# Performance work log

Measured on AMD Instinct MI355X. Metric: run time of the kernel, lower is better.

The kernel has to match this reference:

```python
import jax, jax.numpy as jnp
import numpy as np

B, S, D, H = 2, 2048, 1024, 16
HD = D // H
SCALING = HD ** -0.5


def _length_mask(lengths, seqlen):
    return (jnp.arange(seqlen)[None, :] < jnp.asarray(lengths)[:, None]).astype(jnp.int32)


def setup_inputs() -> dict:
    key = jax.random.key(0)
    ks = jax.random.split(key, 10)
    std = D ** -0.5
    inp = {
        "hidden_states": jax.random.normal(ks[0], (B, S, D), dtype=jnp.float32),
        "Wq": jax.random.normal(ks[1], (D, D), dtype=jnp.float32) * std,
        "bq": jax.random.normal(ks[2], (D,), dtype=jnp.float32) * 0.02,
        "Wk": jax.random.normal(ks[3], (D, D), dtype=jnp.float32) * std,
        "bk": jax.random.normal(ks[4], (D,), dtype=jnp.float32) * 0.02,
        "Wv": jax.random.normal(ks[5], (D, D), dtype=jnp.float32) * std,
        "bv": jax.random.normal(ks[6], (D,), dtype=jnp.float32) * 0.02,
        "Wo": jax.random.normal(ks[7], (D, D), dtype=jnp.float32) * std,
        "bo": jax.random.normal(ks[8], (D,), dtype=jnp.float32) * 0.02,
        # variable valid lengths per batch element (padding at the end)
        "query_mask_1d": _length_mask([S, S - 512], S),
        "key_mask_1d": _length_mask([S, S - 512], S),
    }
    return inp


def reference(hidden_states, Wq, bq, Wk, bk, Wv, bv, Wo, bo, query_mask_1d, key_mask_1d):
    bsz, tgt_len, _ = hidden_states.shape
    # projections (dropout p=0 / eval -> identity)
    q = (hidden_states @ Wq + bq) * SCALING
    k = hidden_states @ Wk + bk
    v = hidden_states @ Wv + bv
    q = q.reshape(bsz, tgt_len, H, HD).transpose(0, 2, 1, 3)  # [B,H,S,HD]
    k = k.reshape(bsz, -1, H, HD).transpose(0, 2, 1, 3)
    v = v.reshape(bsz, -1, H, HD).transpose(0, 2, 1, 3)

    scores = jnp.einsum("bhqd,bhkd->bhqk", q, k)  # [B,H,S,S]
    q_valid = (query_mask_1d != 0)[:, None, :, None]  # [B,1,S,1]
    k_valid = (key_mask_1d != 0)[:, None, None, :]    # [B,1,1,S]
    # masked_fill(-inf) on padded keys; padded-query rows would be all -inf ->
    # softmax NaN -> nan_to_num(0). We compute the same result NaN-free by
    # zeroing the scores of padded-query rows and zeroing their probs after.
    s = jnp.where(k_valid, scores, -jnp.inf)
    s = jnp.where(q_valid, s, 0.0)
    attn_weights = jax.nn.softmax(s, axis=-1) * q_valid  # == softmax + nan_to_num

    attn_output = jnp.einsum("bhqk,bhkd->bhqd", attn_weights, v)
    attn_output = attn_output.transpose(0, 2, 1, 3).reshape(bsz, tgt_len, D)
    attn_output = attn_output @ Wo + bo
    return attn_output
```

## Files before the change

### kernel.cpp

```cpp
#include <hip/hip_runtime.h>
#include <stdint.h>

#define BB 2
#define SS 2048
#define DD 1024
#define HH 16
#define HDIM 64
#define MTOT (BB*SS)
#define QK_SCALE_LOG2E 0.180336880f

typedef unsigned short u16;
typedef __attribute__((ext_vector_type(8))) __bf16 bf16x8;
typedef __attribute__((ext_vector_type(4))) float f32x4;

static __device__ __forceinline__ float exp2_hw(float x) {
    return __builtin_amdgcn_exp2f(x);
}

static __device__ __forceinline__ u16 f2bu(float f) {
    union { float f; uint32_t u; } c; c.f = f;
    uint32_t u = c.u + 0x7fffu + ((c.u >> 16) & 1u);
    return (u16)(u >> 16);
}

static __device__ __forceinline__ u16 f2b_hw(float f) {
    __bf16 b = (__bf16)f;
    union { __bf16 b; u16 u; } c; c.b = b;
    return c.u;
}

static __device__ __forceinline__ uint32_t cvt_pk_bf16(float lo, float hi) {
    uint32_t r;
    asm("v_cvt_pk_bf16_f32 %0, %1, %2" : "=v"(r) : "v"(lo), "v"(hi));
    return r;
}

static __device__ __forceinline__ void gload_lds16(const void* g, void* l) {
    __builtin_amdgcn_global_load_lds(
        (const __attribute__((address_space(1))) uint32_t*)(g),
        (__attribute__((address_space(3))) uint32_t*)(l),
        16, 0, 0);
}

__global__ void k_convert_x(const float* __restrict__ x, u16* __restrict__ xb) {
    int i = (blockIdx.x * blockDim.x + threadIdx.x) * 4;
    float4 v = *(const float4*)(x + i);
    ushort4 o;
    o.x = f2bu(v.x); o.y = f2bu(v.y); o.z = f2bu(v.z); o.w = f2bu(v.w);
    *(ushort4*)(xb + i) = o;
}

__global__ void k_transpose_w(const float* __restrict__ Wq, const float* __restrict__ Wk,
                              const float* __restrict__ Wv, const float* __restrict__ Wo,
                              u16* __restrict__ Wqkv_t, u16* __restrict__ Wo_t) {
    __shared__ float tile[32][33];
    const int which = blockIdx.z;
    const float* W = (which == 0) ? Wq : (which == 1) ? Wk : (which == 2) ? Wv : Wo;
    u16* dst = (which < 3) ? (Wqkv_t + (size_t)which * DD * DD) : Wo_t;
    const int n0 = blockIdx.x * 32, k0 = blockIdx.y * 32;
    const int tx = threadIdx.x, ty = threadIdx.y;
    #pragma unroll
    for (int i = 0; i < 32; i += 8)
        tile[ty + i][tx] = W[(size_t)(k0 + ty + i) * DD + (n0 + tx)];
    __syncthreads();
    #pragma unroll
    for (int i = 0; i < 32; i += 8)
        dst[(size_t)(n0 + ty + i) * DD + (k0 + tx)] = f2bu(tile[tx][ty + i]);
}

#define PH(AP, Q, READB, STAGECODE, TAILWAIT)                                 \
  { bf16x8 afr[2][2];                                                         \
    _Pragma("unroll") for (int m2 = 0; m2 < 2; ++m2)                          \
      _Pragma("unroll") for (int ks = 0; ks < 2; ++ks)                        \
        afr[m2][ks] = rdA(AP, 2*(Q)+m2, ks);                                  \
    if (READB) {                                                              \
      _Pragma("unroll") for (int nf = 0; nf < 3; ++nf)                        \
        _Pragma("unroll") for (int ks = 0; ks < 2; ++ks)                      \
          bfr[nf][ks] = rdB(BP_, nf, ks);                                     \
    }                                                                         \
    STAGECODE;                                                                \
    __builtin_amdgcn_s_barrier();                                             \
    asm volatile("s_waitcnt lgkmcnt(0)" ::: "memory");                        \
    __builtin_amdgcn_sched_barrier(0);                                        \
    __builtin_amdgcn_s_setprio(1);                                            \
    _Pragma("unroll") for (int m2 = 0; m2 < 2; ++m2)                          \
      _Pragma("unroll") for (int nf = 0; nf < 3; ++nf)                        \
        _Pragma("unroll") for (int ks = 0; ks < 2; ++ks)                      \
          acc[2*(Q)+m2][nf] = __builtin_amdgcn_mfma_f32_16x16x32_bf16(        \
              afr[m2][ks], bfr[nf][ks], acc[2*(Q)+m2][nf], 0, 0, 0);          \
    __builtin_amdgcn_s_setprio(0);                                            \
    TAILWAIT;                                                                 \
    __builtin_amdgcn_s_barrier();                                             \
  }

#define QITER(AE, AO, AS2, TB)                                                \
  { const u16* BP_ = Bs0;                                                     \
    PH(AE, 0, true,  { stgA(AS2, 0, (TB)+2); }, {});                          \
    PH(AE, 1, false, { stgA(AS2, 1, (TB)+2); }, {});                          \
    PH(AE, 2, false, { stgB(Bs0, (TB)+2); }, {});                             \
    PH(AE, 3, false, {},                                                      \
       { asm volatile("s_waitcnt vmcnt(7)" ::: "memory"); }); }               \
  { const u16* BP_ = Bs1;                                                     \
    PH(AO, 0, true,  { stgA(AE, 0, (TB)+3); }, {});                           \
    PH(AO, 1, false, { stgA(AE, 1, (TB)+3); }, {});                           \
    PH(AO, 2, false, { stgB(Bs1, (TB)+3); }, {});                             \
    PH(AO, 3, false, {},                                                      \
       { asm volatile("s_waitcnt vmcnt(7)" ::: "memory"); }); }

#define QITERP(AE, AO)                                                        \
  { const u16* BP_ = Bs0;                                                     \
    PH(AE, 0, true,  {}, {});                                                 \
    PH(AE, 1, false, {}, {});                                                 \
    PH(AE, 2, false, {}, {});                                                 \
    PH(AE, 3, false, {},                                                      \
       { asm volatile("s_waitcnt vmcnt(0)" ::: "memory"); }); }               \
  { const u16* BP_ = Bs1;                                                     \
    PH(AO, 0, true,  {}, {});                                                 \
    PH(AO, 1, false, {}, {});                                                 \
    PH(AO, 2, false, {}, {});                                                 \
    PH(AO, 3, false, {}, {}); }

__global__ __launch_bounds__(512, 2) void k_gemm_qkv(
    const u16* __restrict__ Xb, const u16* __restrict__ Wt,
    const float* __restrict__ bq, const float* __restrict__ bk_, const float* __restrict__ bv,
    u16* __restrict__ Qb, u16* __restrict__ Kb, u16* __restrict__ Vt)
{
    __shared__ u16 AsA[3][256 * 64];
    __shared__ u16 BsB[2][192 * 64];

    const int flat = blockIdx.y * 16 + blockIdx.x;
    const int xcd = flat & 7, idx = flat >> 3;
    const int by = ((xcd >> 1) << 2) + (idx >> 3);
    const int bx = ((xcd & 1) << 3) + (idx & 7);
    const int m0 = by << 8, n0 = bx * 192;

    const int t = threadIdx.x;
    const int lane = t & 63, w = t >> 6;
    const int wm = (w >> 2) << 7, wn = (w & 3) * 48;
    const int lr = lane & 15, lg = lane >> 4;

    const u16* Asrc = Xb + (size_t)m0 * DD;
    const u16* Bsrc = Wt + (size_t)n0 * DD;

    f32x4 acc[8][3] = {};
    bf16x8 bfr[3][2];

    auto stgA = [&](u16* bufp, int half, int tt) {
        #pragma unroll
        for (int r = 0; r < 2; ++r) {
            int off = (t + (r << 9)) << 4;
            int row = off >> 7, colb = off & 127;
            int scol = colb ^ ((row & 7) << 4);
            gload_lds16(Asrc + (size_t)((half << 7) + row) * DD + (tt << 6) + (scol >> 1),
                        (char*)bufp + (half << 14) + off);
        }
    };
    auto stgB = [&](u16* bufp, int tt) {
        #pragma unroll
        for (int r = 0; r < 3; ++r) {
            int off = (t + (r << 9)) << 4;
            int row = off >> 7, colb = off & 127;
            int scol = colb ^ ((row & 7) << 4);
            gload_lds16(Bsrc + (size_t)row * DD + (tt << 6) + (scol >> 1),
                        (char*)bufp + off);
        }
    };

    auto rdA = [&](const u16* bufp, int mf, int ks) {
        const int row = wm + (mf << 4) + lr;
        const int col = ((ks << 6) + (lg << 4)) ^ ((row & 7) << 4);
        return *(const bf16x8*)((const char*)bufp + row * 128 + col);
    };
    auto rdB = [&](const u16* bufp, int nf, int ks) {
        const int row = wn + (nf << 4) + lr;
        const int col = ((ks << 6) + (lg << 4)) ^ ((row & 7) << 4);
        return *(const bf16x8*)((const char*)bufp + row * 128 + col);
    };

    u16* pA0 = AsA[0]; u16* pA1 = AsA[1]; u16* pA2 = AsA[2];
    u16* Bs0 = BsB[0]; u16* Bs1 = BsB[1];

    stgA(pA0, 0, 0); stgA(pA0, 1, 0); stgB(Bs0, 0);
    stgA(pA1, 0, 1); stgA(pA1, 1, 1); stgB(Bs1, 1);
    asm volatile("s_waitcnt vmcnt(7)" ::: "memory");
    __builtin_amdgcn_sched_barrier(0);
    __builtin_amdgcn_s_barrier();

    #pragma unroll 1
    for (int j = 0; j < 2; ++j) {
        const int tb = j * 6;
        QITER(pA0, pA1, pA2, tb);
        QITER(pA2, pA0, pA1, tb + 2);
        QITER(pA1, pA2, pA0, tb + 4);
    }
    QITER(pA0, pA1, pA2, 12);
    QITERP(pA2, pA0);

    #pragma unroll
    for (int mf = 0; mf < 8; ++mf) {
        #pragma unroll
        for (int nf = 0; nf < 3; ++nf) {
            const int n = n0 + wn + (nf << 4) + lr;
            const int mbase = m0 + wm + (mf << 4) + (lg << 2);
            const int b_ = mbase >> 11;
            const int s_ = mbase & 2047;
            const int seg = n >> 10;
            const int nn = n & 1023;
            const int hh = nn >> 6, d = nn & 63;
            if (seg == 0) {
                const float bias = bq[nn];
                u16* dstp = Qb + (((size_t)b_ * HH + hh) * SS + s_) * HDIM + d;
                #pragma unroll
                for (int r = 0; r < 4; ++r)
                    dstp[(size_t)r * HDIM] = f2bu((acc[mf][nf][r] + bias) * QK_SCALE_LOG2E);
            } else if (seg == 1) {
                const float bias = bk_[nn];
                u16* dstp = Kb + (((size_t)b_ * HH + hh) * SS + s_) * HDIM + d;
                #pragma unroll
                for (int r = 0; r < 4; ++r)
                    dstp[(size_t)r * HDIM] = f2bu(acc[mf][nf][r] + bias);
            } else {
                const float bias = bv[nn];
                ushort4 pk;
                pk.x = f2bu(acc[mf][nf][0] + bias);
                pk.y = f2bu(acc[mf][nf][1] + bias);
                pk.z = f2bu(acc[mf][nf][2] + bias);
                pk.w = f2bu(acc[mf][nf][3] + bias);
                *(ushort4*)(Vt + (((size_t)b_ * HH + hh) * HDIM + d) * SS + s_) = pk;
            }
        }
    }
}

__global__ __launch_bounds__(512, 4) void k_attn(
    const u16* __restrict__ Qb, const u16* __restrict__ Kb, const u16* __restrict__ Vt,
    const int* __restrict__ qmask, const int* __restrict__ kmask,
    u16* __restrict__ X2)
{
    const int i = blockIdx.x;
    const int xcd = i & 7, j = i >> 3;
    const int qt = j & 15;
    const int bh = xcd + ((j >> 4) << 3);
    const int b_ = bh >> 4;
    const int h = bh & 15;

    const int t = threadIdx.x;
    const int lane = t & 63, w = t >> 6;
    const int lr = lane & 15, lg = lane >> 4;

    __shared__ u16 Ks[3][64 * 64];
    __shared__ u16 Vs[3][64 * 64];
    __shared__ u16 Ps[8][16 * 64];

    const int q0 = qt << 7;
    const size_t bhs = (size_t)b_ * HH + h;
    const u16* Qbase = Qb + bhs * SS * HDIM;
    const char* KbaseB = (const char*)(Kb + bhs * SS * HDIM);
    const char* VbaseB = (const char*)(Vt + bhs * HDIM * SS);

    if (qmask[b_ * SS + q0] == 0) {
        #pragma unroll
        for (int r = 0; r < 4; ++r) {
            const int q = q0 + (w << 4) + (lg << 2) + r;
            #pragma unroll
            for (int nf = 0; nf < 4; ++nf)
                X2[((size_t)b_ * SS + q) * DD + (h << 6) + (nf << 4) + lr] = 0;
        }
        return;
    }

    int kv = (lane < 32) ? kmask[b_ * SS + (lane << 6)] : 0;
    unsigned long long bal = __ballot(kv != 0);
    const int nkt = __popcll(bal);

    bf16x8 qf[2];
    #pragma unroll
    for (int ks = 0; ks < 2; ++ks)
        qf[ks] = *(const bf16x8*)(Qbase + (size_t)(q0 + (w << 4) + lr) * HDIM + (ks << 5) + (lg << 3));

    bf16x8 vones;
    #pragma unroll
    for (int i2 = 0; i2 < 8; ++i2) vones[i2] = (__bf16)1.0f;

    f32x4 o[4] = {};
    f32x4 lacc = {};

    auto stage = [&](int buf, int kb) {
        const int off = t << 4;
        const int row = off >> 7, colb = off & 127;
        const int scol = colb ^ ((row & 7) << 4);
        gload_lds16(KbaseB + (size_t)(kb + row) * 128 + scol, (char*)Ks[buf] + off);
        gload_lds16(VbaseB + ((size_t)row * SS + (size_t)kb) * 2 + scol, (char*)Vs[buf] + off);
    };

    if (nkt > 0) stage(0, 0);
    if (nkt > 1) stage(1, 64);
    if (nkt > 1) { asm volatile("s_waitcnt vmcnt(2)" ::: "memory"); }
    else         { asm volatile("s_waitcnt vmcnt(0)" ::: "memory"); }
    __builtin_amdgcn_sched_barrier(0);
    __builtin_amdgcn_s_barrier();

    u16* P = Ps[w];

    int cur = 0;
    #pragma unroll 1
    for (int kt = 0; kt < nkt; ++kt) {
        const int kb = kt << 6;
        const int nxt = (cur == 2) ? 0 : cur + 1;
        const int nx2 = (nxt == 2) ? 0 : nxt + 1;
        if (kt + 2 < nkt) stage(nx2, kb + 128);

        f32x4 sf[4] = {};
        __builtin_amdgcn_s_setprio(1);
        #pragma unroll
        for (int ks = 0; ks < 2; ++ks) {
            #pragma unroll
            for (int f = 0; f < 4; ++f) {
                const int krow = (f << 4) + lr;
                const int kcol = ((ks << 6) + (lg << 4)) ^ ((krow & 7) << 4);
                bf16x8 kf = *(const bf16x8*)((const char*)Ks[cur] + krow * 128 + kcol);
                sf[f] = __builtin_amdgcn_mfma_f32_16x16x32_bf16(kf, qf[ks], sf[f], 0, 0, 0);
            }
        }
        __builtin_amdgcn_s_setprio(0);
        if (kt == nkt - 1) {
            #pragma unroll
            for (int f = 0; f < 4; ++f) {
                #pragma unroll
                for (int r = 0; r < 4; ++r) {
                    if (kmask[b_ * SS + kb + (f << 4) + (lg << 2) + r] == 0)
                        sf[f][r] = -1e30f;
                }
            }
        }
        #pragma unroll
        for (int f = 0; f < 4; ++f)
            #pragma unroll
            for (int r = 0; r < 4; ++r)
                sf[f][r] = exp2_hw(sf[f][r]);

        #pragma unroll
        for (int f = 0; f < 4; ++f) {
            uint2 pk;
            pk.x = cvt_pk_bf16(sf[f][0], sf[f][1]);
            pk.y = cvt_pk_bf16(sf[f][2], sf[f][3]);
            *(uint2*)((char*)P + (((lr << 7) + (f << 5) + (lg << 3)) ^ ((lr & 7) << 4))) = pk;
        }

        __builtin_amdgcn_s_setprio(1);
        #pragma unroll
        for (int ks = 0; ks < 2; ++ks) {
            bf16x8 pa = *(const bf16x8*)((const char*)P + (((lr << 7) + (ks << 6) + (lg << 4)) ^ ((lr & 7) << 4)));
            lacc = __builtin_amdgcn_mfma_f32_16x16x32_bf16(pa, vones, lacc, 0, 0, 0);
            #pragma unroll
            for (int nf = 0; nf < 4; ++nf) {
                const int vrow = (nf << 4) + lr;
                const int vcol = ((ks << 6) + (lg << 4)) ^ ((vrow & 7) << 4);
                bf16x8 vb = *(const bf16x8*)((const char*)Vs[cur] + vrow * 128 + vcol);
                o[nf] = __builtin_amdgcn_mfma_f32_16x16x32_bf16(pa, vb, o[nf], 0, 0, 0);
            }
        }
        __builtin_amdgcn_s_setprio(0);

        if (kt + 2 < nkt) { asm volatile("s_waitcnt vmcnt(2)" ::: "memory"); }
        else              { asm volatile("s_waitcnt vmcnt(0)" ::: "memory"); }
        __builtin_amdgcn_sched_barrier(0);
        __builtin_amdgcn_s_barrier();
        cur = nxt;
    }

    #pragma unroll
    for (int r = 0; r < 4; ++r) {
        const int q = q0 + (w << 4) + (lg << 2) + r;
        float l = lacc[r];
        float inv = (l > 0.f) ? __builtin_amdgcn_rcpf(l) : 0.f;
        if (qmask[b_ * SS + q] == 0) inv = 0.f;
        #pragma unroll
        for (int nf = 0; nf < 4; ++nf)
            X2[((size_t)b_ * SS + q) * DD + (h << 6) + (nf << 4) + lr] = f2b_hw(o[nf][r] * inv);
    }
}

__global__ __launch_bounds__(256) void k_gemm_out(
    const u16* __restrict__ X2, const u16* __restrict__ Wot,
    const float* __restrict__ bo, float* __restrict__ out)
{
    __shared__ u16 As2[2][128 * 64];
    __shared__ u16 Bs2[2][128 * 64];
    const int m0 = blockIdx.y * 128, n0 = blockIdx.x * 128;
    const int t = threadIdx.x;
    const int lane = t & 63, w = t >> 6;
    const int wm = (w >> 1) << 6, wn = (w & 1) << 6;
    const int lr = lane & 15, lg = lane >> 4;

    f32x4 acc[4][4] = {};

    auto stage = [&](int buf, int k0) {
        #pragma unroll
        for (int i = 0; i < 4; ++i) {
            int off = (t + (i << 8)) << 4;
            int row = off >> 7, colb = off & 127;
            int scol = colb ^ ((row & 7) << 4);
            gload_lds16(X2 + (size_t)(m0 + row) * DD + k0 + (scol >> 1), (char*)As2[buf] + off);
            gload_lds16(Wot + (size_t)(n0 + row) * DD + k0 + (scol >> 1), (char*)Bs2[buf] + off);
        }
    };

    stage(0, 0);
    __syncthreads();

    int cur = 0;
    for (int kt = 0; kt < 16; ++kt) {
        if (kt < 15) stage(cur ^ 1, (kt + 1) << 6);
        #pragma unroll
        for (int ks = 0; ks < 2; ++ks) {
            bf16x8 a[4], b[4];
            #pragma unroll
            for (int i = 0; i < 4; ++i) {
                const int row = wm + (i << 4) + lr;
                a[i] = *(const bf16x8*)((const char*)As2[cur] + row * 128 + (((ks << 6) + (lg << 4)) ^ ((row & 7) << 4)));
            }
            #pragma unroll
            for (int i = 0; i < 4; ++i) {
                const int row = wn + (i << 4) + lr;
                b[i] = *(const bf16x8*)((const char*)Bs2[cur] + row * 128 + (((ks << 6) + (lg << 4)) ^ ((row & 7) << 4)));
            }
            #pragma unroll
            for (int mi = 0; mi < 4; ++mi)
                #pragma unroll
                for (int ni = 0; ni < 4; ++ni)
                    acc[mi][ni] = __builtin_amdgcn_mfma_f32_16x16x32_bf16(a[mi], b[ni], acc[mi][ni], 0, 0, 0);
        }
        __syncthreads();
        cur ^= 1;
    }

    #pragma unroll
    for (int mi = 0; mi < 4; ++mi) {
        #pragma unroll
        for (int ni = 0; ni < 4; ++ni) {
            const int n = n0 + wn + (ni << 4) + lr;
            const int mbase = m0 + wm + (mi << 4) + (lg << 2);
            const float bias = bo[n];
            #pragma unroll
            for (int r = 0; r < 4; ++r)
                out[(size_t)(mbase + r) * DD + n] = acc[mi][ni][r] + bias;
        }
    }
}

extern "C" void kernel_launch(void* const* d_in, const int* in_sizes, int n_in,
                              void* d_out, int out_size, void* d_ws, size_t ws_size,
                              hipStream_t stream) {
    const float* hs = (const float*)d_in[0];
    const float* Wq = (const float*)d_in[1];
    const float* bq = (const float*)d_in[2];
    const float* Wk = (const float*)d_in[3];
    const float* bk = (const float*)d_in[4];
    const float* Wv = (const float*)d_in[5];
    const float* bv = (const float*)d_in[6];
    const float* Wo = (const float*)d_in[7];
    const float* bo = (const float*)d_in[8];
    const int* qm = (const int*)d_in[9];
    const int* km = (const int*)d_in[10];
    float* out = (float*)d_out;

    char* ws = (char*)d_ws;
    const size_t MB = 1024 * 1024;
    u16* Xb  = (u16*)(ws + 0);
    u16* Wt3 = (u16*)(ws + 8 * MB);
    u16* Wot = (u16*)(ws + 14 * MB);
    u16* Qb  = (u16*)(ws + 16 * MB);
    u16* Kb  = (u16*)(ws + 24 * MB);
    u16* Vt  = (u16*)(ws + 32 * MB);
    u16* X2  = (u16*)(ws + 40 * MB);

    k_convert_x<<<dim3(MTOT * DD / 1024), dim3(256), 0, stream>>>(hs, Xb);
    k_transpose_w<<<dim3(32, 32, 4), dim3(32, 8), 0, stream>>>(Wq, Wk, Wv, Wo, Wt3, Wot);
    k_gemm_qkv<<<dim3(16, 16), dim3(512), 0, stream>>>(Xb, Wt3, bq, bk, bv, Qb, Kb, Vt);
    k_attn<<<dim3(512), dim3(512), 0, stream>>>(Qb, Kb, Vt, qm, km, X2);
    k_gemm_out<<<dim3(8, 32), dim3(256), 0, stream>>>(X2, Wot, bo, out);
}
```

Before: 113.0 us.

## Give each attention wave 32 query rows with 256-thread blocks

```diff
diff --git a/kernel.cpp b/kernel.cpp
--- a/kernel.cpp
+++ b/kernel.cpp
@@ -196,6 +196,7 @@
     QITER(pA0, pA1, pA2, 12);
     QITERP(pA2, pA0);
 
+    const int whichseg = n0 >> 10; (void)whichseg;
     #pragma unroll
     for (int mf = 0; mf < 8; ++mf) {
         #pragma unroll
@@ -232,7 +233,7 @@
     }
 }
 
-__global__ __launch_bounds__(512, 4) void k_attn(
+__global__ __launch_bounds__(256, 2) void k_attn(
     const u16* __restrict__ Qb, const u16* __restrict__ Kb, const u16* __restrict__ Vt,
     const int* __restrict__ qmask, const int* __restrict__ kmask,
     u16* __restrict__ X2)
@@ -250,7 +251,7 @@
 
     __shared__ u16 Ks[3][64 * 64];
     __shared__ u16 Vs[3][64 * 64];
-    __shared__ u16 Ps[8][16 * 64];
+    __shared__ u16 Ps[4][32 * 64];
 
     const int q0 = qt << 7;
     const size_t bhs = (size_t)b_ * HH + h;
@@ -260,12 +261,14 @@
 
     if (qmask[b_ * SS + q0] == 0) {
         #pragma unroll
-        for (int r = 0; r < 4; ++r) {
-            const int q = q0 + (w << 4) + (lg << 2) + r;
-            #pragma unroll
-            for (int nf = 0; nf < 4; ++nf)
-                X2[((size_t)b_ * SS + q) * DD + (h << 6) + (nf << 4) + lr] = 0;
-        }
+        for (int qh = 0; qh < 2; ++qh)
+            #pragma unroll
+            for (int r = 0; r < 4; ++r) {
+                const int q = q0 + (w << 5) + (qh << 4) + (lg << 2) + r;
+                #pragma unroll
+                for (int nf = 0; nf < 4; ++nf)
+                    X2[((size_t)b_ * SS + q) * DD + (h << 6) + (nf << 4) + lr] = 0;
+            }
         return;
     }
 
@@ -273,29 +276,34 @@
     unsigned long long bal = __ballot(kv != 0);
     const int nkt = __popcll(bal);
 
-    bf16x8 qf[2];
-    #pragma unroll
-    for (int ks = 0; ks < 2; ++ks)
-        qf[ks] = *(const bf16x8*)(Qbase + (size_t)(q0 + (w << 4) + lr) * HDIM + (ks << 5) + (lg << 3));
+    bf16x8 qf[2][2];
+    #pragma unroll
+    for (int qh = 0; qh < 2; ++qh)
+        #pragma unroll
+        for (int ks = 0; ks < 2; ++ks)
+            qf[qh][ks] = *(const bf16x8*)(Qbase + (size_t)(q0 + (w << 5) + (qh << 4) + lr) * HDIM + (ks << 5) + (lg << 3));
 
     bf16x8 vones;
     #pragma unroll
     for (int i2 = 0; i2 < 8; ++i2) vones[i2] = (__bf16)1.0f;
 
-    f32x4 o[4] = {};
-    f32x4 lacc = {};
+    f32x4 o[2][4] = {};
+    f32x4 lacc[2] = {};
 
     auto stage = [&](int buf, int kb) {
-        const int off = t << 4;
-        const int row = off >> 7, colb = off & 127;
-        const int scol = colb ^ ((row & 7) << 4);
-        gload_lds16(KbaseB + (size_t)(kb + row) * 128 + scol, (char*)Ks[buf] + off);
-        gload_lds16(VbaseB + ((size_t)row * SS + (size_t)kb) * 2 + scol, (char*)Vs[buf] + off);
+        #pragma unroll
+        for (int r2 = 0; r2 < 2; ++r2) {
+            const int off = (t + (r2 << 8)) << 4;
+            const int row = off >> 7, colb = off & 127;
+            const int scol = colb ^ ((row & 7) << 4);
+            gload_lds16(KbaseB + (size_t)(kb + row) * 128 + scol, (char*)Ks[buf] + off);
+            gload_lds16(VbaseB + ((size_t)row * SS + (size_t)kb) * 2 + scol, (char*)Vs[buf] + off);
+        }
     };
 
     if (nkt > 0) stage(0, 0);
     if (nkt > 1) stage(1, 64);
-    if (nkt > 1) { asm volatile("s_waitcnt vmcnt(2)" ::: "memory"); }
+    if (nkt > 1) { asm volatile("s_waitcnt vmcnt(4)" ::: "memory"); }
     else         { asm volatile("s_waitcnt vmcnt(0)" ::: "memory"); }
     __builtin_amdgcn_sched_barrier(0);
     __builtin_amdgcn_s_barrier();
@@ -310,7 +318,7 @@
         const int nx2 = (nxt == 2) ? 0 : nxt + 1;
         if (kt + 2 < nkt) stage(nx2, kb + 128);
 
-        f32x4 sf[4] = {};
+        f32x4 sf[2][4] = {};
         __builtin_amdgcn_s_setprio(1);
         #pragma unroll
         for (int ks = 0; ks < 2; ++ks) {
@@ -319,7 +327,8 @@
                 const int krow = (f << 4) + lr;
                 const int kcol = ((ks << 6) + (lg << 4)) ^ ((krow & 7) << 4);
                 bf16x8 kf = *(const bf16x8*)((const char*)Ks[cur] + krow * 128 + kcol);
-                sf[f] = __builtin_amdgcn_mfma_f32_16x16x32_bf16(kf, qf[ks], sf[f], 0, 0, 0);
+                sf[0][f] = __builtin_amdgcn_mfma_f32_16x16x32_bf16(kf, qf[0][ks], sf[0][f], 0, 0, 0);
+                sf[1][f] = __builtin_amdgcn_mfma_f32_16x16x32_bf16(kf, qf[1][ks], sf[1][f], 0, 0, 0);
             }
         }
         __builtin_amdgcn_s_setprio(0);
@@ -328,41 +337,55 @@
             for (int f = 0; f < 4; ++f) {
                 #pragma unroll
                 for (int r = 0; r < 4; ++r) {
-                    if (kmask[b_ * SS + kb + (f << 4) + (lg << 2) + r] == 0)
-                        sf[f][r] = -1e30f;
+                    if (kmask[b_ * SS + kb + (f << 4) + (lg << 2) + r] == 0) {
+                        sf[0][f][r] = -1e30f;
+                        sf[1][f][r] = -1e30f;
+                    }
                 }
             }
         }
         #pragma unroll
-        for (int f = 0; f < 4; ++f)
-            #pragma unroll
-            for (int r = 0; r < 4; ++r)
-                sf[f][r] = exp2_hw(sf[f][r]);
-
-        #pragma unroll
-        for (int f = 0; f < 4; ++f) {
-            uint2 pk;
-            pk.x = cvt_pk_bf16(sf[f][0], sf[f][1]);
-            pk.y = cvt_pk_bf16(sf[f][2], sf[f][3]);
-            *(uint2*)((char*)P + (((lr << 7) + (f << 5) + (lg << 3)) ^ ((lr & 7) << 4))) = pk;
+        for (int qh = 0; qh < 2; ++qh)
+            #pragma unroll
+            for (int f = 0; f < 4; ++f)
+                #pragma unroll
+                for (int r = 0; r < 4; ++r)
+                    sf[qh][f][r] = exp2_hw(sf[qh][f][r]);
+
+        #pragma unroll
+        for (int qh = 0; qh < 2; ++qh) {
+            const int rq = (qh << 4) + lr;
+            #pragma unroll
+            for (int f = 0; f < 4; ++f) {
+                uint2 pk;
+                pk.x = cvt_pk_bf16(sf[qh][f][0], sf[qh][f][1]);
+                pk.y = cvt_pk_bf16(sf[qh][f][2], sf[qh][f][3]);
+                *(uint2*)((char*)P + (((rq << 7) + (f << 5) + (lg << 3)) ^ ((rq & 7) << 4))) = pk;
+            }
         }
 
         __builtin_amdgcn_s_setprio(1);
         #pragma unroll
         for (int ks = 0; ks < 2; ++ks) {
-            bf16x8 pa = *(const bf16x8*)((const char*)P + (((lr << 7) + (ks << 6) + (lg << 4)) ^ ((lr & 7) << 4)));
-            lacc = __builtin_amdgcn_mfma_f32_16x16x32_bf16(pa, vones, lacc, 0, 0, 0);
+            bf16x8 pa[2];
+            #pragma unroll
+            for (int qh = 0; qh < 2; ++qh) {
+                const int rq = (qh << 4) + lr;
+                pa[qh] = *(const bf16x8*)((const char*)P + (((rq << 7) + (ks << 6) + (lg << 4)) ^ ((rq & 7) << 4)));
+                lacc[qh] = __builtin_amdgcn_mfma_f32_16x16x32_bf16(pa[qh], vones, lacc[qh], 0, 0, 0);
+            }
             #pragma unroll
             for (int nf = 0; nf < 4; ++nf) {
                 const int vrow = (nf << 4) + lr;
                 const int vcol = ((ks << 6) + (lg << 4)) ^ ((vrow & 7) << 4);
                 bf16x8 vb = *(const bf16x8*)((const char*)Vs[cur] + vrow * 128 + vcol);
-                o[nf] = __builtin_amdgcn_mfma_f32_16x16x32_bf16(pa, vb, o[nf], 0, 0, 0);
+                o[0][nf] = __builtin_amdgcn_mfma_f32_16x16x32_bf16(pa[0], vb, o[0][nf], 0, 0, 0);
+                o[1][nf] = __builtin_amdgcn_mfma_f32_16x16x32_bf16(pa[1], vb, o[1][nf], 0, 0, 0);
             }
         }
         __builtin_amdgcn_s_setprio(0);
 
-        if (kt + 2 < nkt) { asm volatile("s_waitcnt vmcnt(2)" ::: "memory"); }
+        if (kt + 2 < nkt) { asm volatile("s_waitcnt vmcnt(4)" ::: "memory"); }
         else              { asm volatile("s_waitcnt vmcnt(0)" ::: "memory"); }
         __builtin_amdgcn_sched_barrier(0);
         __builtin_amdgcn_s_barrier();
@@ -370,15 +393,17 @@
     }
 
     #pragma unroll
-    for (int r = 0; r < 4; ++r) {
-        const int q = q0 + (w << 4) + (lg << 2) + r;
-        float l = lacc[r];
-        float inv = (l > 0.f) ? __builtin_amdgcn_rcpf(l) : 0.f;
-        if (qmask[b_ * SS + q] == 0) inv = 0.f;
-        #pragma unroll
-        for (int nf = 0; nf < 4; ++nf)
-            X2[((size_t)b_ * SS + q) * DD + (h << 6) + (nf << 4) + lr] = f2b_hw(o[nf][r] * inv);
-    }
+    for (int qh = 0; qh < 2; ++qh)
+        #pragma unroll
+        for (int r = 0; r < 4; ++r) {
+            const int q = q0 + (w << 5) + (qh << 4) + (lg << 2) + r;
+            float l = lacc[qh][r];
+            float inv = (l > 0.f) ? __builtin_amdgcn_rcpf(l) : 0.f;
+            if (qmask[b_ * SS + q] == 0) inv = 0.f;
+            #pragma unroll
+            for (int nf = 0; nf < 4; ++nf)
+                X2[((size_t)b_ * SS + q) * DD + (h << 6) + (nf << 4) + lr] = f2b_hw(o[qh][nf][r] * inv);
+        }
 }
 
 __global__ __launch_bounds__(256) void k_gemm_out(
@@ -478,6 +503,6 @@
     k_convert_x<<<dim3(MTOT * DD / 1024), dim3(256), 0, stream>>>(hs, Xb);
     k_transpose_w<<<dim3(32, 32, 4), dim3(32, 8), 0, stream>>>(Wq, Wk, Wv, Wo, Wt3, Wot);
     k_gemm_qkv<<<dim3(16, 16), dim3(512), 0, stream>>>(Xb, Wt3, bq, bk, bv, Qb, Kb, Vt);
-    k_attn<<<dim3(512), dim3(512), 0, stream>>>(Qb, Kb, Vt, qm, km, X2);
+    k_attn<<<dim3(512), dim3(256), 0, stream>>>(Qb, Kb, Vt, qm, km, X2);
     k_gemm_out<<<dim3(8, 32), dim3(256), 0, stream>>>(X2, Wot, bo, out);
 }
```

After: 114.9 us. Within noise of the previous version (+1.7%).
